# Performance work log

Hardware: AMD Instinct MI355X
Metric: run time of the kernel (lower is better)

Reference implementation:

```python
import jax, jax.numpy as jnp
import numpy as np

B = 32768      # number of graphs in the batch
NPG = 54       # nodes per graph (fixed by reshape(batch_size, 54*4))
EPG = 144      # directed edges per graph (Catan board: 72 undirected)
N = B * NPG
E = B * EPG
GLOB = 10


def _lin(k, fan_in, fan_out):
    lim = 1.0 / np.sqrt(fan_in)
    kw, kb = jax.random.split(k)
    W = jax.random.uniform(kw, (fan_in, fan_out), jnp.float32, -lim, lim)
    b = jax.random.uniform(kb, (fan_out,), jnp.float32, -lim, lim)
    return W, b


def setup_inputs() -> dict:
    key = jax.random.key(0)
    ks = jax.random.split(key, 16)
    x = jax.random.normal(ks[0], (N, 8), jnp.float32)
    # PyG-style batched edge_index: edges stay within each 54-node block
    base = (jnp.arange(B, dtype=jnp.int32) * NPG)[:, None]
    src = (jax.random.randint(ks[1], (B, EPG), 0, NPG, jnp.int32) + base).reshape(-1)
    dst = (jax.random.randint(ks[2], (B, EPG), 0, NPG, jnp.int32) + base).reshape(-1)
    edge_index = jnp.stack([src, dst], axis=0)
    edge_attr = jax.random.uniform(ks[3], (E,), jnp.float32)
    globalFeats = jax.random.normal(ks[4], (B, GLOB), jnp.float32)
    # GraphConv 1: in=8 -> hidden=16  (lin_rel has bias, lin_root has no bias)
    W_rel1, b1 = _lin(ks[5], 8, 16)
    W_root1, _ = _lin(ks[6], 8, 16)
    # GraphConv 2: 16 -> 4
    W_rel2, b2 = _lin(ks[7], 16, 4)
    W_root2, _ = _lin(ks[8], 16, 4)
    # Global MLP: 10 -> 8 -> 8 -> 10
    Wg1, bg1 = _lin(ks[9], GLOB, 8)
    Wg2, bg2 = _lin(ks[10], 8, 8)
    Wg3, bg3 = _lin(ks[11], 8, GLOB)
    # Out MLP: 54*4 + 10 = 226 -> 128 -> 1
    Wo1, bo1 = _lin(ks[12], NPG * 4 + GLOB, 128)
    Wo2, bo2 = _lin(ks[13], 128, 1)
    return dict(x=x, edge_index=edge_index, edge_attr=edge_attr,
                globalFeats=globalFeats,
                W_rel1=W_rel1, b1=b1, W_root1=W_root1,
                W_rel2=W_rel2, b2=b2, W_root2=W_root2,
                Wg1=Wg1, bg1=bg1, Wg2=Wg2, bg2=bg2, Wg3=Wg3, bg3=bg3,
                Wo1=Wo1, bo1=bo1, Wo2=Wo2, bo2=bo2, isTrain=0)


def _graph_conv(x, src, dst, edge_attr, W_rel, b, W_root):
    # PyG GraphConv (aggr='add'): out = lin_rel(sum_j w_ij * x_j) + lin_root(x)
    msg = edge_attr[:, None] * x[src]                       # [E, F_in]
    agg = jax.ops.segment_sum(msg, dst, num_segments=N)     # [N, F_in]
    return agg @ W_rel + b + x @ W_root


def reference(x, edge_index, edge_attr, globalFeats,
              W_rel1, b1, W_root1, W_rel2, b2, W_root2,
              Wg1, bg1, Wg2, bg2, Wg3, bg3, Wo1, bo1, Wo2, bo2, isTrain):
    src, dst = edge_index[0], edge_index[1]
    h = jax.nn.relu(_graph_conv(x, src, dst, edge_attr, W_rel1, b1, W_root1))
    h = jax.nn.relu(_graph_conv(h, src, dst, edge_attr, W_rel2, b2, W_root2))
    embeds = h.reshape(B, NPG * 4)                          # [B, 216]
    g = jax.nn.relu(globalFeats @ Wg1 + bg1)
    g = jax.nn.relu(g @ Wg2 + bg2)
    g = jax.nn.relu(g @ Wg3 + bg3)
    out = jnp.concatenate([embeds, g], axis=-1)             # [B, 226]
    # dropout p=0.2 with isTrain=0 (eval) -> identity
    out = jax.nn.relu(out @ Wo1 + bo1)
    out = jax.nn.sigmoid(out @ Wo2 + bo2)                   # [B, 1]
    return out
```

## Files before the change

### kernel.cpp

```cpp
#include <hip/hip_runtime.h>
#include <hip/hip_fp16.h>
#include <math.h>

#define NPG 54
#define EPG 144
#define GLOB 10
#define VROW 216
#define GPB 2

typedef _Float16 f16x8 __attribute__((ext_vector_type(8)));
typedef _Float16 f16x4 __attribute__((ext_vector_type(4)));
typedef float    f32x4 __attribute__((ext_vector_type(4)));

#define WSYNC() asm volatile("s_waitcnt lgkmcnt(0)" ::: "memory")

struct __align__(16) GL {
    _Float16 Adj[NPG][72];
    _Float16 XH[16][72];
};

__global__ __launch_bounds__(128, 4) void graph_kernel(
    const float* __restrict__ x,
    const int*   __restrict__ edge_index,
    const float* __restrict__ edge_attr,
    const float* __restrict__ W_rel1, const float* __restrict__ b1,
    const float* __restrict__ W_root1,
    const float* __restrict__ W_rel2, const float* __restrict__ b2,
    const float* __restrict__ W_root2,
    _Float16* __restrict__ v_out,
    int E_total)
{
    __shared__ GL S[GPB];
    const int tid  = threadIdx.x;
    const int w    = tid >> 6;
    const int lane = tid & 63;
    const int ln15 = lane & 15;
    const int quad = lane >> 4;
    const int g    = blockIdx.x * GPB + w;
    GL& L = S[w];
    const int nbase = g * NPG;
    const int ebase = g * EPG;

    _Float16 (*cat)[40] = (_Float16(*)[40])&L.Adj[0][0];

    int   esrc_r[3], edst_r[3];
    float ea_r[3];
    #pragma unroll
    for (int k = 0; k < 3; k++) {
        int e = lane + 64 * k;
        if (e < EPG) {
            esrc_r[k] = edge_index[ebase + e] - nbase;
            edst_r[k] = edge_index[(size_t)E_total + ebase + e] - nbase;
            ea_r[k]   = edge_attr[ebase + e];
        } else { esrc_r[k] = 0; edst_r[k] = -1; ea_r[k] = 0.0f; }
    }
    f16x8 xv = {0, 0, 0, 0, 0, 0, 0, 0};
    if (lane < NPG) {
        const float4* xg4 = (const float4*)(x + (size_t)(nbase + lane) * 8);
        float4 lo = xg4[0], hi = xg4[1];
        xv = (f16x8){ (_Float16)lo.x, (_Float16)lo.y, (_Float16)lo.z, (_Float16)lo.w,
                      (_Float16)hi.x, (_Float16)hi.y, (_Float16)hi.z, (_Float16)hi.w };
    }

    f16x8 wf1 = {0, 0, 0, 0, 0, 0, 0, 0};
    if (quad == 0) {
        #pragma unroll
        for (int j = 0; j < 8; j++) wf1[j] = (_Float16)W_rel1[j * 16 + ln15];
    } else if (quad == 1) {
        #pragma unroll
        for (int j = 0; j < 8; j++) wf1[j] = (_Float16)W_root1[j * 16 + ln15];
    }
    f16x8 wf2 = {0, 0, 0, 0, 0, 0, 0, 0};
    if (ln15 < 4) {
        #pragma unroll
        for (int j = 0; j < 8; j++) {
            int k = quad * 8 + j;
            wf2[j] = (_Float16)((k < 16) ? W_rel2[k * 4 + ln15]
                                         : W_root2[(k - 16) * 4 + ln15]);
        }
    }
    const float b1v = b1[ln15];
    const float b2v = b2[ln15 & 3];

    {
        uint4* z = (uint4*)&L;
        #pragma unroll
        for (int i = lane; i < 630; i += 64) z[i] = make_uint4(0, 0, 0, 0);
    }
    if (lane < NPG) {
        #pragma unroll
        for (int f = 0; f < 8; f++) L.XH[f][lane] = xv[f];
    }
    WSYNC();

    #pragma unroll
    for (int k = 0; k < 3; k++) {
        if (edst_r[k] >= 0) {
            int s = esrc_r[k];
            __half2* cell = (__half2*)&L.Adj[edst_r[k]][s & ~1];
            __half a16 = __float2half(ea_r[k]);
            __half z16 = __float2half(0.0f);
            __half2 val = (s & 1) ? __halves2half2(z16, a16)
                                  : __halves2half2(a16, z16);
            unsafeAtomicAdd(cell, val);
        }
    }
    WSYNC();

    f16x8 af[4][2];
    #pragma unroll
    for (int t = 0; t < 4; t++)
        #pragma unroll
        for (int ks = 0; ks < 2; ks++)
            af[t][ks] = *(const f16x8*)&L.Adj[t * 16 + ln15][ks * 32 + quad * 8];
    WSYNC();

    if (lane < NPG) *(f16x8*)&cat[lane][8] = xv;

    f32x4 acc1[4];
    #pragma unroll
    for (int t = 0; t < 4; t++) acc1[t] = (f32x4){0.f, 0.f, 0.f, 0.f};
    #pragma unroll
    for (int ks = 0; ks < 2; ks++) {
        f16x8 bx = *(const f16x8*)&L.XH[ln15][ks * 32 + quad * 8];
        #pragma unroll
        for (int t = 0; t < 4; t++)
            acc1[t] = __builtin_amdgcn_mfma_f32_16x16x32_f16(af[t][ks], bx, acc1[t], 0, 0, 0);
    }
    #pragma unroll
    for (int t = 0; t < 4; t++)
        #pragma unroll
        for (int r = 0; r < 4; r++)
            if (ln15 < 8) cat[t * 16 + quad * 4 + r][ln15] = (_Float16)acc1[t][r];
    WSYNC();

    f32x4 accL[4];
    #pragma unroll
    for (int t = 0; t < 4; t++) {
        f16x8 al = *(const f16x8*)&cat[t * 16 + ln15][quad * 8];
        f32x4 ci = (f32x4){b1v, b1v, b1v, b1v};
        accL[t] = __builtin_amdgcn_mfma_f32_16x16x32_f16(al, wf1, ci, 0, 0, 0);
    }
    #pragma unroll
    for (int t = 0; t < 4; t++) {
        f16x4 hp;
        #pragma unroll
        for (int r = 0; r < 4; r++) {
            int node = t * 16 + quad * 4 + r;
            float h = (node < NPG) ? fmaxf(accL[t][r], 0.0f) : 0.0f;
            hp[r] = (_Float16)h;
            cat[node][16 + ln15] = (_Float16)h;
        }
        *(f16x4*)&L.XH[ln15][t * 16 + quad * 4] = hp;
    }
    WSYNC();

    f32x4 acc2[4];
    #pragma unroll
    for (int t = 0; t < 4; t++) acc2[t] = (f32x4){0.f, 0.f, 0.f, 0.f};
    #pragma unroll
    for (int ks = 0; ks < 2; ks++) {
        f16x8 bh = *(const f16x8*)&L.XH[ln15][ks * 32 + quad * 8];
        #pragma unroll
        for (int t = 0; t < 4; t++)
            acc2[t] = __builtin_amdgcn_mfma_f32_16x16x32_f16(af[t][ks], bh, acc2[t], 0, 0, 0);
    }
    #pragma unroll
    for (int t = 0; t < 4; t++)
        #pragma unroll
        for (int r = 0; r < 4; r++)
            cat[t * 16 + quad * 4 + r][ln15] = (_Float16)acc2[t][r];
    WSYNC();

    _Float16* vt = &L.XH[0][0];
    #pragma unroll
    for (int t = 0; t < 4; t++) {
        f16x8 a2 = *(const f16x8*)&cat[t * 16 + ln15][quad * 8];
        f32x4 ci = (f32x4){b2v, b2v, b2v, b2v};
        f32x4 h2 = __builtin_amdgcn_mfma_f32_16x16x32_f16(a2, wf2, ci, 0, 0, 0);
        #pragma unroll
        for (int r = 0; r < 4; r++) {
            int node = t * 16 + quad * 4 + r;
            if (ln15 < 4 && node < NPG)
                vt[node * 4 + ln15] = (_Float16)fmaxf(h2[r], 0.0f);
        }
    }
    WSYNC();

    if (lane < 27)
        *(f16x8*)(v_out + (size_t)g * VROW + lane * 8) = *(const f16x8*)&vt[lane * 8];
}

#define BTS 264

__global__ __launch_bounds__(512) void out_mlp_mfma(
    const _Float16* __restrict__ V,
    const float* __restrict__ gf,
    const float* __restrict__ Wg1, const float* __restrict__ bg1,
    const float* __restrict__ Wg2, const float* __restrict__ bg2,
    const float* __restrict__ Wg3, const float* __restrict__ bg3,
    const float* __restrict__ Wo1,
    const float* __restrict__ bo1,
    const float* __restrict__ Wo2,
    const float* __restrict__ bo2,
    float* __restrict__ out)
{
    extern __shared__ _Float16 Bt[];

    const int tid  = threadIdx.x;
    const int w    = tid >> 6;
    const int lane = tid & 63;
    const int ln15 = lane & 15;
    const int quad = lane >> 4;
    const int row0 = blockIdx.x * 128;
    const int row  = row0 + w * 16 + ln15;

    float bo1v[8], wo2v[8];
    #pragma unroll
    for (int t = 0; t < 8; t++) {
        bo1v[t] = bo1[t * 16 + ln15];
        wo2v[t] = Wo2[t * 16 + ln15];
    }
    const float bo2v = bo2[0];

    float t3[GLOB];
    {
        const float* gr = gf + (size_t)row * GLOB;
        float t0[GLOB];
        #pragma unroll
        for (int i = 0; i < GLOB; i++) t0[i] = gr[i];
        float t1[8];
        #pragma unroll
        for (int j = 0; j < 8; j++) {
            float a = bg1[j];
            #pragma unroll
            for (int i = 0; i < GLOB; i++) a += t0[i] * Wg1[i * 8 + j];
            t1[j] = fmaxf(a, 0.0f);
        }
        float t2[8];
        #pragma unroll
        for (int j = 0; j < 8; j++) {
            float a = bg2[j];
            #pragma unroll
            for (int i = 0; i < 8; i++) a += t1[i] * Wg2[i * 8 + j];
            t2[j] = fmaxf(a, 0.0f);
        }
        #pragma unroll
        for (int j = 0; j < GLOB; j++) {
            float a = bg3[j];
            #pragma unroll
            for (int i = 0; i < 8; i++) a += t2[i] * Wg3[i * GLOB + j];
            t3[j] = fmaxf(a, 0.0f);
        }
    }

    const _Float16* Arow = V + (size_t)row * VROW;
    f16x8 af[8];
    #pragma unroll
    for (int s = 0; s < 6; s++)
        af[s] = *(const f16x8*)(Arow + s * 32 + quad * 8);
    if (quad == 3)
        af[6] = (f16x8){ (_Float16)t3[0], (_Float16)t3[1], (_Float16)t3[2], (_Float16)t3[3],
                         (_Float16)t3[4], (_Float16)t3[5], (_Float16)t3[6], (_Float16)t3[7] };
    else
        af[6] = *(const f16x8*)(Arow + 192 + quad * 8);
    af[7] = (f16x8){0, 0, 0, 0, 0, 0, 0, 0};
    if (quad == 0) { af[7][0] = (_Float16)t3[8]; af[7][1] = (_Float16)t3[9]; }

    {
        int4* bz = (int4*)Bt;
        for (int i = tid; i < 4224; i += 512)
            bz[i] = make_int4(0, 0, 0, 0);
    }
    __syncthreads();
    for (int i = tid; i < 7232; i += 512) {
        int k  = i >> 5;
        int nq = (i & 31) * 4;
        float4 v = *(const float4*)(Wo1 + (size_t)k * 128 + nq);
        Bt[(nq + 0) * BTS + k] = (_Float16)v.x;
        Bt[(nq + 1) * BTS + k] = (_Float16)v.y;
        Bt[(nq + 2) * BTS + k] = (_Float16)v.z;
        Bt[(nq + 3) * BTS + k] = (_Float16)v.w;
    }
    __syncthreads();

    f32x4 acc[8];
    #pragma unroll
    for (int t = 0; t < 8; t++) acc[t] = (f32x4){0.f, 0.f, 0.f, 0.f};

    for (int s = 0; s < 8; s++) {
        #pragma unroll
        for (int t = 0; t < 8; t++) {
            f16x8 bf = *(const f16x8*)&Bt[(t * 16 + ln15) * BTS + s * 32 + quad * 8];
            acc[t] = __builtin_amdgcn_mfma_f32_16x16x32_f16(af[s], bf, acc[t], 0, 0, 0);
        }
    }

    #pragma unroll
    for (int rr = 0; rr < 4; rr++) {
        float p = 0.0f;
        #pragma unroll
        for (int t = 0; t < 8; t++) {
            float h = fmaxf(acc[t][rr] + bo1v[t], 0.0f);
            p += h * wo2v[t];
        }
        p += __shfl_xor(p, 1);
        p += __shfl_xor(p, 2);
        p += __shfl_xor(p, 4);
        p += __shfl_xor(p, 8);
        if (ln15 == rr) {
            int orow = row0 + w * 16 + quad * 4 + rr;
            out[orow] = 1.0f / (1.0f + expf(-(p + bo2v)));
        }
    }
}

extern "C" void kernel_launch(void* const* d_in, const int* in_sizes, int n_in,
                              void* d_out, int out_size, void* d_ws, size_t ws_size,
                              hipStream_t stream) {
    const float* x        = (const float*)d_in[0];
    const int*   ei       = (const int*)  d_in[1];
    const float* ea       = (const float*)d_in[2];
    const float* gf       = (const float*)d_in[3];
    const float* W_rel1   = (const float*)d_in[4];
    const float* b1       = (const float*)d_in[5];
    const float* W_root1  = (const float*)d_in[6];
    const float* W_rel2   = (const float*)d_in[7];
    const float* b2       = (const float*)d_in[8];
    const float* W_root2  = (const float*)d_in[9];
    const float* Wg1      = (const float*)d_in[10];
    const float* bg1      = (const float*)d_in[11];
    const float* Wg2      = (const float*)d_in[12];
    const float* bg2      = (const float*)d_in[13];
    const float* Wg3      = (const float*)d_in[14];
    const float* bg3      = (const float*)d_in[15];
    const float* Wo1      = (const float*)d_in[16];
    const float* bo1      = (const float*)d_in[17];
    const float* Wo2      = (const float*)d_in[18];
    const float* bo2      = (const float*)d_in[19];

    float* out   = (float*)d_out;
    _Float16* V  = (_Float16*)d_ws;

    const int B = out_size;
    const int E = in_sizes[1] / 2;

    graph_kernel<<<B / GPB, 128, 0, stream>>>(
        x, ei, ea,
        W_rel1, b1, W_root1, W_rel2, b2, W_root2,
        V, E);

    out_mlp_mfma<<<B / 128, 512, 128 * BTS * sizeof(_Float16), stream>>>(
        V, gf, Wg1, bg1, Wg2, bg2, Wg3, bg3, Wo1, bo1, Wo2, bo2, out);
}
```

Before: 219.7 us.

## Pretranspose Wo1 to fp16 in graph kernel and read it directly from global

The first 128 blocks of the graph kernel now transpose and convert Wo1 into a zero-padded fp16 [128][256] buffer in workspace. The output MLP no longer stages Wo1 into LDS per block; it loads B fragments straight from global/L2. Block size is halved to 256 threads with twice as many blocks. This removes a large per-block LDS fill and its barriers, at the cost of more global/L2 traffic for B fragments and extra work in the graph kernel.

```diff
diff --git a/kernel.cpp b/kernel.cpp
--- a/kernel.cpp
+++ b/kernel.cpp
@@ -27,6 +27,8 @@
     const float* __restrict__ W_root1,
     const float* __restrict__ W_rel2, const float* __restrict__ b2,
     const float* __restrict__ W_root2,
+    const float* __restrict__ Wo1,
+    _Float16* __restrict__ wo1t,
     _Float16* __restrict__ v_out,
     int E_total)
 {
@@ -43,6 +45,15 @@
 
     _Float16 (*cat)[40] = (_Float16(*)[40])&L.Adj[0][0];
 
+    if (blockIdx.x < 128) {
+        int n = blockIdx.x;
+        int k = tid;
+        wo1t[n * 256 + k] = (_Float16)Wo1[(size_t)k * 128 + n];
+        int k2 = tid + 128;
+        float v1 = (k2 < 226) ? Wo1[(size_t)k2 * 128 + n] : 0.0f;
+        wo1t[n * 256 + k2] = (_Float16)v1;
+    }
+
     int   esrc_r[3], edst_r[3];
     float ea_r[3];
     #pragma unroll
@@ -191,29 +202,24 @@
         *(f16x8*)(v_out + (size_t)g * VROW + lane * 8) = *(const f16x8*)&vt[lane * 8];
 }
 
-#define BTS 264
-
-__global__ __launch_bounds__(512) void out_mlp_mfma(
+__global__ __launch_bounds__(256) void out_mlp_mfma(
     const _Float16* __restrict__ V,
+    const _Float16* __restrict__ Wo1t,
     const float* __restrict__ gf,
     const float* __restrict__ Wg1, const float* __restrict__ bg1,
     const float* __restrict__ Wg2, const float* __restrict__ bg2,
     const float* __restrict__ Wg3, const float* __restrict__ bg3,
-    const float* __restrict__ Wo1,
     const float* __restrict__ bo1,
     const float* __restrict__ Wo2,
     const float* __restrict__ bo2,
     float* __restrict__ out)
 {
-    extern __shared__ _Float16 Bt[];
-
     const int tid  = threadIdx.x;
     const int w    = tid >> 6;
-    const int lane = tid & 63;
-    const int ln15 = lane & 15;
-    const int quad = lane >> 4;
-    const int row0 = blockIdx.x * 128;
-    const int row  = row0 + w * 16 + ln15;
+    const int ln15 = tid & 15;
+    const int quad = (tid & 63) >> 4;
+    const int rowbase = blockIdx.x * 64 + w * 16;
+    const int row  = rowbase + ln15;
 
     float bo1v[8], wo2v[8];
     #pragma unroll
@@ -267,33 +273,19 @@
     af[7] = (f16x8){0, 0, 0, 0, 0, 0, 0, 0};
     if (quad == 0) { af[7][0] = (_Float16)t3[8]; af[7][1] = (_Float16)t3[9]; }
 
-    {
-        int4* bz = (int4*)Bt;
-        for (int i = tid; i < 4224; i += 512)
-            bz[i] = make_int4(0, 0, 0, 0);
-    }
-    __syncthreads();
-    for (int i = tid; i < 7232; i += 512) {
-        int k  = i >> 5;
-        int nq = (i & 31) * 4;
-        float4 v = *(const float4*)(Wo1 + (size_t)k * 128 + nq);
-        Bt[(nq + 0) * BTS + k] = (_Float16)v.x;
-        Bt[(nq + 1) * BTS + k] = (_Float16)v.y;
-        Bt[(nq + 2) * BTS + k] = (_Float16)v.z;
-        Bt[(nq + 3) * BTS + k] = (_Float16)v.w;
-    }
-    __syncthreads();
-
     f32x4 acc[8];
     #pragma unroll
     for (int t = 0; t < 8; t++) acc[t] = (f32x4){0.f, 0.f, 0.f, 0.f};
 
+    #pragma unroll
     for (int s = 0; s < 8; s++) {
-        #pragma unroll
-        for (int t = 0; t < 8; t++) {
-            f16x8 bf = *(const f16x8*)&Bt[(t * 16 + ln15) * BTS + s * 32 + quad * 8];
-            acc[t] = __builtin_amdgcn_mfma_f32_16x16x32_f16(af[s], bf, acc[t], 0, 0, 0);
-        }
+        f16x8 bf[8];
+        #pragma unroll
+        for (int t = 0; t < 8; t++)
+            bf[t] = *(const f16x8*)(Wo1t + ((t * 16 + ln15) << 8) + s * 32 + quad * 8);
+        #pragma unroll
+        for (int t = 0; t < 8; t++)
+            acc[t] = __builtin_amdgcn_mfma_f32_16x16x32_f16(af[s], bf[t], acc[t], 0, 0, 0);
     }
 
     #pragma unroll
@@ -309,7 +301,7 @@
         p += __shfl_xor(p, 4);
         p += __shfl_xor(p, 8);
         if (ln15 == rr) {
-            int orow = row0 + w * 16 + quad * 4 + rr;
+            int orow = rowbase + quad * 4 + rr;
             out[orow] = 1.0f / (1.0f + expf(-(p + bo2v)));
         }
     }
@@ -340,16 +332,18 @@
     const float* bo2      = (const float*)d_in[19];
 
     float* out   = (float*)d_out;
-    _Float16* V  = (_Float16*)d_ws;
 
     const int B = out_size;
     const int E = in_sizes[1] / 2;
+
+    _Float16* V    = (_Float16*)d_ws;
+    _Float16* Wo1t = (_Float16*)((char*)d_ws + (size_t)B * VROW * 2);
 
     graph_kernel<<<B / GPB, 128, 0, stream>>>(
         x, ei, ea,
         W_rel1, b1, W_root1, W_rel2, b2, W_root2,
-        V, E);
-
-    out_mlp_mfma<<<B / 128, 512, 128 * BTS * sizeof(_Float16), stream>>>(
-        V, gf, Wg1, bg1, Wg2, bg2, Wg3, bg3, Wo1, bo1, Wo2, bo2, out);
+        Wo1, Wo1t, V, E);
+
+    out_mlp_mfma<<<B / 64, 256, 0, stream>>>(
+        V, Wo1t, gf, Wg1, bg1, Wg2, bg2, Wg3, bg3, bo1, Wo2, bo2, out);
 }
```

New measurement: 224.7 us. 1.02x slower.
